# Kernel optimization log

Measured on AMD Instinct MI355X. Metric: run time of the kernel, lower is better.

Reference implementation:

```python
import jax, jax.numpy as jnp
import numpy as np

B = 256; M = 6; H = 448; INC = 448; EMB = 32; NHEAD = 8; DFF = 2048
OBS = 20; HOR = 30
D = EMB + 4 * NHEAD + INC      # transformer d_model = 512 (requires INC == hidden_dim)
LBUF = OBS + HOR               # 50-token buffer; index 49 is written but never read
HD = D // NHEAD
FUS_IN = D + 7 + INC           # fusion layer input = 71 + 2*hidden_dim


def _ln(x, g, b):
    mu = x.mean(-1, keepdims=True)
    var = ((x - mu) ** 2).mean(-1, keepdims=True)
    return (x - mu) * jax.lax.rsqrt(var + 1e-5) * g + b


def setup_inputs() -> dict:
    key = jax.random.key(0)
    ks = jax.random.split(key, 16)
    s = jnp.float32(0.02)
    n = lambda i, shp: jax.random.normal(ks[i], shp, dtype=jnp.float32)
    return {
        "feat_in": n(0, (B, 1, INC)),
        "loc_in": n(1, (B, M, 2)),
        "obs_trajs": n(2, (OBS, B, 2)),
        "W_emb": n(3, (2, EMB)) * s, "b_emb": jnp.zeros((EMB,)),
        "W_qkv": n(4, (D, 3 * D)) * s, "b_qkv": jnp.zeros((3 * D,)),
        "W_o": n(5, (D, D)) * s, "b_o": jnp.zeros((D,)),
        "W_ff1": n(6, (D, DFF)) * s, "b_ff1": jnp.zeros((DFF,)),
        "W_ff2": n(7, (DFF, D)) * s, "b_ff2": jnp.zeros((D,)),
        "ln1_g": jnp.ones((D,)), "ln1_b": jnp.zeros((D,)),
        "ln2_g": jnp.ones((D,)), "ln2_b": jnp.zeros((D,)),
        "W_fus": n(8, (FUS_IN, H)) * s, "b_fus": jnp.zeros((H,)),
        "W_out": n(9, (H, 2)) * s, "b_out": jnp.zeros((2,)),
    }


def reference(feat_in, loc_in, obs_trajs, W_emb, b_emb, W_qkv, b_qkv, W_o, b_o,
              W_ff1, b_ff1, W_ff2, b_ff2, ln1_g, ln1_b, ln2_g, ln2_b,
              W_fus, b_fus, W_out, b_out):
    feat = feat_in[:, 0]                                     # [B, INC]
    emb_obs = jax.nn.relu(obs_trajs @ W_emb + b_emb)         # [OBS, B, EMB]
    pos0 = jnp.zeros((LBUF, B, 2), feat.dtype).at[:OBS].set(obs_trajs)
    emb0 = jnp.zeros((LBUF, B, EMB), feat.dtype).at[:OBS].set(emb_obs)
    idxs = jnp.arange(OBS, OBS + HOR)
    scale = 1.0 / jnp.sqrt(jnp.float32(HD))
    rep = NHEAD // 2

    def run_sample(goal):                                    # goal: [B, 2]
        def step(carry, frame_idx):
            pos, emb = carry
            last = pos[frame_idx - 1]                        # [B, 2]
            dist = goal - last
            tcol = jnp.zeros((B, 1), feat.dtype) + frame_idx
            # order matches torch.cat: (emb, goal, last, dist, time, feat)
            extras = jnp.concatenate([jnp.tile(goal, (1, rep)), jnp.tile(last, (1, rep)),
                                      jnp.tile(dist, (1, rep)), jnp.tile(tcol, (1, NHEAD))], -1)
            x = jnp.concatenate([emb,
                                 jnp.broadcast_to(extras, (LBUF, B, 4 * NHEAD)),
                                 jnp.broadcast_to(feat, (LBUF, B, INC))], -1)   # [LBUF, B, D]
            qkv = x @ W_qkv + b_qkv
            q, k, v = jnp.split(qkv, 3, axis=-1)
            qh = q[frame_idx - 1].reshape(B, NHEAD, HD)      # only last query needed
            kh = k.reshape(LBUF, B, NHEAD, HD)
            vh = v.reshape(LBUF, B, NHEAD, HD)
            scores = jnp.einsum('bhd,lbhd->bhl', qh, kh) * scale
            valid = jnp.arange(LBUF) < frame_idx             # tokens 0..frame_idx-1 exist
            scores = jnp.where(valid[None, None, :], scores, -1e9)
            attn = jax.nn.softmax(scores, axis=-1)
            ctx = jnp.einsum('bhl,lbhd->bhd', attn, vh).reshape(B, D)
            a = ctx @ W_o + b_o
            x_last = x[frame_idx - 1]
            h1 = _ln(x_last + a, ln1_g, ln1_b)               # post-LN encoder layer (eval, no dropout)
            ff = jax.nn.relu(h1 @ W_ff1 + b_ff1) @ W_ff2 + b_ff2
            h2 = _ln(h1 + ff, ln2_g, ln2_b)
            fus = jnp.concatenate([h2, last, goal, dist, tcol, feat], -1)       # [B, FUS_IN]
            out = (fus @ W_fus + b_fus) @ W_out + b_out                         # [B, 2]
            pos = pos.at[frame_idx].set(out)
            emb = emb.at[frame_idx].set(jax.nn.relu(out @ W_emb + b_emb))
            return (pos, emb), out
        _, ys = jax.lax.scan(step, (pos0, emb0), idxs)
        return ys                                            # [HOR, B, 2]

    ys = jax.vmap(run_sample, in_axes=1)(loc_in)             # [M, HOR, B, 2]
    return ys.transpose(2, 0, 1, 3).reshape(B, M, HOR * 2)
```

## Files before the change

### kernel.cpp

```cpp
#include <hip/hip_runtime.h>
#include <math.h>

#define B_   256
#define N_   1536
#define OBS_ 20
#define HOR_ 30

typedef __bf16 bf16;
typedef bf16  bf16x8 __attribute__((ext_vector_type(8)));
typedef float f32x4  __attribute__((ext_vector_type(4)));

__global__ __launch_bounds__(256) void gemm_k(
    const float* __restrict__ A, int lda,
    const float* __restrict__ Bw, int ldb,
    float* __restrict__ C, bf16* __restrict__ Cb, int ldc,
    int K, const float* __restrict__ colBias)
{
    __shared__ float As[16][68];
    __shared__ float Bs[16][68];
    const int tid = threadIdx.x;
    const int tx = tid & 15, ty = tid >> 4;
    const int n0 = blockIdx.y * 64, j0 = blockIdx.x * 64;
    float acc[4][4] = {};
    const int a_kk = tid & 15, a_nn0 = tid >> 4;
    const int b_jj = tid & 63, b_kk0 = tid >> 6;
    for (int k0 = 0; k0 < K; k0 += 16) {
#pragma unroll
        for (int i = 0; i < 4; i++) {
            int nn = a_nn0 + 16 * i;
            As[a_kk][nn] = (k0 + a_kk < K) ? A[(size_t)(n0 + nn) * lda + k0 + a_kk] : 0.f;
        }
#pragma unroll
        for (int i = 0; i < 4; i++) {
            int kk = b_kk0 + 4 * i;
            Bs[kk][b_jj] = (k0 + kk < K) ? Bw[(size_t)(k0 + kk) * ldb + j0 + b_jj] : 0.f;
        }
        __syncthreads();
#pragma unroll
        for (int kk = 0; kk < 16; kk++) {
            float4 av = *(const float4*)&As[kk][ty * 4];
            float4 bv = *(const float4*)&Bs[kk][tx * 4];
            float aa[4] = {av.x, av.y, av.z, av.w};
            float bb[4] = {bv.x, bv.y, bv.z, bv.w};
#pragma unroll
            for (int i = 0; i < 4; i++)
#pragma unroll
                for (int j = 0; j < 4; j++) acc[i][j] += aa[i] * bb[j];
        }
        __syncthreads();
    }
#pragma unroll
    for (int i = 0; i < 4; i++) {
        int n = n0 + ty * 4 + i;
#pragma unroll
        for (int j = 0; j < 4; j++) {
            int jj = j0 + tx * 4 + j;
            float v = acc[i][j];
            if (colBias) v += colBias[jj];
            if (C)  C[(size_t)n * ldc + jj] = v;
            if (Cb) Cb[(size_t)n * ldc + jj] = (bf16)v;
        }
    }
}

__global__ void pack_k(const float* __restrict__ srcF, const bf16* __restrict__ srcB,
                       int srcRows, int KC, int J, int lds, bf16* __restrict__ dst)
{
    int idx = blockIdx.x * 256 + threadIdx.x;
    int total = (J / 16) * KC * 64;
    if (idx >= total) return;
    int lane = idx & 63;
    int kc = (idx >> 6) % KC;
    int jg = idx / (64 * KC);
    int k0 = kc * 32 + (lane >> 4) * 8;
    int col = jg * 16 + (lane & 15);
    bf16x8 v;
#pragma unroll
    for (int i = 0; i < 8; i++) {
        int r = k0 + i;
        float x = 0.f;
        if (r < srcRows) x = srcF ? srcF[(size_t)r * lds + col] : (float)srcB[(size_t)r * lds + col];
        v[i] = (bf16)x;
    }
    *(bf16x8*)&dst[(size_t)idx * 8] = v;
}

template<int KC>
__global__ __launch_bounds__(256) void fgemm_k(
    const bf16* __restrict__ A, int lda,
    const bf16* __restrict__ Bp,
    float* __restrict__ C, bf16* __restrict__ Cb, int ldc,
    const float* __restrict__ colBias,
    const float* __restrict__ rowMat, int ldRm,
    int doRelu)
{
    const int n0 = blockIdx.y * 32;
    const int j0g = blockIdx.x * 4;
    const int tid = threadIdx.x;
    const int w = tid >> 6, lane = tid & 63;
    const int quad = lane >> 4, m15 = lane & 15;
    const int r0 = (w & 1) * 16;
    const int cg = (w >> 1) * 2;
    const bf16* Arow = &A[(size_t)(n0 + r0 + m15) * lda + quad * 8];
    const bf16* B0 = &Bp[((size_t)(j0g + cg) * KC * 64 + lane) * 8];
    const bf16* B1 = &Bp[((size_t)(j0g + cg + 1) * KC * 64 + lane) * 8];
    f32x4 acc0 = {}, acc1 = {};
#pragma unroll 8
    for (int kc = 0; kc < KC; kc++) {
        bf16x8 af = *(const bf16x8*)&Arow[kc * 32];
        bf16x8 b0 = *(const bf16x8*)&B0[(size_t)kc * 512];
        bf16x8 b1 = *(const bf16x8*)&B1[(size_t)kc * 512];
        acc0 = __builtin_amdgcn_mfma_f32_16x16x32_bf16(af, b0, acc0, 0, 0, 0);
        acc1 = __builtin_amdgcn_mfma_f32_16x16x32_bf16(af, b1, acc1, 0, 0, 0);
    }
#pragma unroll
    for (int g = 0; g < 2; g++) {
        f32x4 a = g ? acc1 : acc0;
        int j = (j0g + cg + g) * 16 + m15;
        float cb = colBias ? colBias[j] : 0.f;
#pragma unroll
        for (int r = 0; r < 4; r++) {
            int n = n0 + r0 + quad * 4 + r;
            float v = a[r] + cb;
            if (rowMat) v += rowMat[(size_t)(n / 6) * ldRm + j];
            if (doRelu) v = fmaxf(v, 0.f);
            if (C)  C[(size_t)n * ldc + j] = v;
            if (Cb) Cb[(size_t)n * ldc + j] = (bf16)v;
        }
    }
}

__global__ __launch_bounds__(256) void emb_obs_k(
    const float* __restrict__ obs, const float* __restrict__ Wemb,
    const float* __restrict__ bemb, float* __restrict__ emb_obs)
{
    int tid = blockIdx.x * 256 + threadIdx.x;
    if (tid >= OBS_ * B_ * 32) return;
    int r = tid >> 5, e = tid & 31;
    float v = obs[r * 2] * Wemb[e] + obs[r * 2 + 1] * Wemb[32 + e] + bemb[e];
    emb_obs[tid] = fmaxf(v, 0.f);
}

__global__ __launch_bounds__(256) void weff_k(
    const float* __restrict__ Wqkv, const float* __restrict__ bqkv,
    float* __restrict__ Weff, float* __restrict__ WeffT)
{
    __shared__ float qrow[512];
    const int r = blockIdx.x;
    const int t = threadIdx.x;
    for (int j = t; j < 512; j += 256)
        qrow[j] = (r < 512) ? Wqkv[(size_t)r * 1536 + j] : bqkv[j];
    __syncthreads();
    const int h = t >> 5, c = t & 31;
    float acc = 0.f;
#pragma unroll 8
    for (int d = 0; d < 64; d++)
        acc += qrow[h * 64 + d] * Wqkv[(size_t)c * 1536 + 512 + h * 64 + d];
    Weff[(size_t)r * 256 + t] = acc;
    if (r < 64) WeffT[(size_t)t * 64 + r] = acc;
}

__global__ __launch_bounds__(256) void wov_k(
    const float* __restrict__ Wqkv, const float* __restrict__ Wo,
    bf16* __restrict__ WovCat)
{
    __shared__ float vrow[64];
    const int row = blockIdx.x;
    const int h = row >> 5, c = row & 31;
    const int t = threadIdx.x;
    if (t < 64) vrow[t] = Wqkv[(size_t)c * 1536 + 1024 + h * 64 + t];
    __syncthreads();
    for (int j = t; j < 512; j += 256) {
        float acc = 0.f;
#pragma unroll 8
        for (int d = 0; d < 64; d++)
            acc += vrow[d] * Wo[(size_t)(h * 64 + d) * 512 + j];
        WovCat[(size_t)row * 512 + j] = (bf16)acc;
    }
}

__global__ __launch_bounds__(256) void attn_k(
    const float* __restrict__ qp, const float* __restrict__ emb_obs,
    const float* __restrict__ emb_gen, bf16* __restrict__ ecA1b, int t)
{
    __shared__ float qp_s[256];
    __shared__ float emb_s[50 * 33];
    __shared__ float at_s[4][64];
    const int n = blockIdx.x, b = n / 6, tid = threadIdx.x;
    qp_s[tid] = qp[(size_t)n * 256 + tid];
    for (int idx = tid; idx < t * 32; idx += 256) {
        int l = idx >> 5, c = idx & 31;
        emb_s[l * 33 + c] = (l < OBS_) ? emb_obs[((size_t)l * B_ + b) * 32 + c]
                                       : emb_gen[((size_t)(l - OBS_) * N_ + n) * 32 + c];
    }
    __syncthreads();
    const int w = tid >> 6, lane = tid & 63;
#pragma unroll
    for (int hh = 0; hh < 2; hh++) {
        const int h = w * 2 + hh;
        float sc = -1e30f;
        if (lane < t) {
            float s_ = 0.f;
#pragma unroll 8
            for (int c = 0; c < 32; c++) s_ += emb_s[lane * 33 + c] * qp_s[h * 32 + c];
            sc = s_ * 0.125f;
        }
        float mx = sc;
#pragma unroll
        for (int o = 32; o > 0; o >>= 1) mx = fmaxf(mx, __shfl_xor(mx, o, 64));
        float e = (lane < t) ? __expf(sc - mx) : 0.f;
        float sm = e;
#pragma unroll
        for (int o = 32; o > 0; o >>= 1) sm += __shfl_xor(sm, o, 64);
        at_s[w][lane] = e / sm;
        if (lane < 32) {
            float ec = 0.f;
            for (int l = 0; l < t; l++) ec += at_s[w][l] * emb_s[l * 33 + lane];
            ecA1b[(size_t)n * 288 + h * 32 + lane] = (bf16)ec;
        }
    }
}

__global__ __launch_bounds__(512) void aln1_k(
    const bf16* __restrict__ A,
    const bf16* __restrict__ Bp,
    const float* __restrict__ featvO,
    const float* __restrict__ A1f,
    const float* __restrict__ feat,
    const float* __restrict__ g, const float* __restrict__ bt,
    float* __restrict__ h1f, bf16* __restrict__ h1b)
{
    __shared__ float redS[8][16];
    __shared__ float redQ[8][16];
    const int n0 = blockIdx.x * 16;
    const int tid = threadIdx.x;
    const int w = tid >> 6, lane = tid & 63;
    const int quad = lane >> 4, m15 = lane & 15;
    const bf16* Arow = &A[(size_t)(n0 + m15) * 288 + quad * 8];
    const bf16* Bb = &Bp[((size_t)(w * 4) * 9 * 64 + lane) * 8];
    f32x4 acc[4] = {};
#pragma unroll 3
    for (int kc = 0; kc < 9; kc++) {
        bf16x8 af = *(const bf16x8*)&Arow[kc * 32];
#pragma unroll
        for (int gi = 0; gi < 4; gi++) {
            bf16x8 bg = *(const bf16x8*)&Bb[(size_t)gi * 9 * 64 * 8 + (size_t)kc * 512];
            acc[gi] = __builtin_amdgcn_mfma_f32_16x16x32_bf16(af, bg, acc[gi], 0, 0, 0);
        }
    }
    float vv[4][4];
    float sS[4] = {}, sQ[4] = {};
#pragma unroll
    for (int gi = 0; gi < 4; gi++) {
        int j = (w * 4 + gi) * 16 + m15;
#pragma unroll
        for (int r = 0; r < 4; r++) {
            int n = n0 + quad * 4 + r;
            int b = n / 6;
            float x = (j < 64) ? A1f[(size_t)n * 64 + j] : feat[(size_t)b * 448 + (j - 64)];
            float v = acc[gi][r] + featvO[(size_t)b * 512 + j] + x;
            vv[gi][r] = v; sS[r] += v; sQ[r] += v * v;
        }
    }
#pragma unroll
    for (int o = 1; o < 16; o <<= 1) {
#pragma unroll
        for (int r = 0; r < 4; r++) { sS[r] += __shfl_xor(sS[r], o, 64); sQ[r] += __shfl_xor(sQ[r], o, 64); }
    }
    if (m15 == 0) {
#pragma unroll
        for (int r = 0; r < 4; r++) { redS[w][quad * 4 + r] = sS[r]; redQ[w][quad * 4 + r] = sQ[r]; }
    }
    __syncthreads();
    float mu[4], rs[4];
#pragma unroll
    for (int r = 0; r < 4; r++) {
        int row = quad * 4 + r;
        float s = 0.f, q = 0.f;
#pragma unroll
        for (int ww = 0; ww < 8; ww++) { s += redS[ww][row]; q += redQ[ww][row]; }
        mu[r] = s * (1.f / 512.f);
        float var = q * (1.f / 512.f) - mu[r] * mu[r];
        rs[r] = rsqrtf(var + 1e-5f);
    }
#pragma unroll
    for (int gi = 0; gi < 4; gi++) {
        int j = (w * 4 + gi) * 16 + m15;
        float gj = g[j], bj = bt[j];
#pragma unroll
        for (int r = 0; r < 4; r++) {
            int n = n0 + quad * 4 + r;
            float vn = (vv[gi][r] - mu[r]) * rs[r] * gj + bj;
            h1f[(size_t)n * 512 + j] = vn;
            h1b[(size_t)n * 512 + j] = (bf16)vn;
        }
    }
}

__global__ __launch_bounds__(256) void fusfin_k(
    const float* __restrict__ h1f, const float* __restrict__ ffB,
    const float* __restrict__ g2, const float* __restrict__ bt2,
    float* __restrict__ small5,
    const bf16* __restrict__ Bp,
    const float* __restrict__ feat_fus,
    const float* __restrict__ Wout, const float* __restrict__ bout,
    const float* __restrict__ Wemb, const float* __restrict__ bemb,
    const float* __restrict__ loc,
    const float* __restrict__ WeffT,
    const float* __restrict__ featqp,
    float* __restrict__ dout, float* __restrict__ emb_gen,
    float* __restrict__ A1f, bf16* __restrict__ ecA1b,
    float* __restrict__ qp, int s)
{
    __shared__ __attribute__((aligned(16))) bf16 h2s[16][552];
    __shared__ float red0[4][16], red1[4][16];
    __shared__ float osh[16][2];
    __shared__ __attribute__((aligned(16))) float A1s[16][64];
    const int n0 = blockIdx.x * 16;
    const int tid = threadIdx.x;

    {
        const int row = tid >> 4, li = tid & 15;
        const int n = n0 + row;
        float v32[32];
        float s_ = 0.f, sq = 0.f;
        const float* h1p = &h1f[(size_t)n * 512 + li * 32];
        const float* ffp = &ffB[(size_t)n * 512 + li * 32];
#pragma unroll
        for (int i4 = 0; i4 < 8; i4++) {
            float4 a4 = *(const float4*)&h1p[i4 * 4];
            float4 b4 = *(const float4*)&ffp[i4 * 4];
            float x0 = a4.x + b4.x, x1 = a4.y + b4.y, x2 = a4.z + b4.z, x3 = a4.w + b4.w;
            v32[i4 * 4 + 0] = x0; v32[i4 * 4 + 1] = x1; v32[i4 * 4 + 2] = x2; v32[i4 * 4 + 3] = x3;
            s_ += x0 + x1 + x2 + x3;
            sq += x0 * x0 + x1 * x1 + x2 * x2 + x3 * x3;
        }
#pragma unroll
        for (int o = 1; o < 16; o <<= 1) { s_ += __shfl_xor(s_, o, 64); sq += __shfl_xor(sq, o, 64); }
        float mu = s_ * (1.f / 512.f);
        float var = sq * (1.f / 512.f) - mu * mu;
        float rs = rsqrtf(var + 1e-5f);
#pragma unroll
        for (int i = 0; i < 32; i++) {
            int c = li * 32 + i;
            float vn = (v32[i] - mu) * rs * g2[c] + bt2[c];
            h2s[row][c] = (bf16)vn;
        }
        if (li == 0) {
#pragma unroll
            for (int sl = 0; sl < 32; sl++) {
                float vt = (sl < 7) ? small5[(size_t)n * 8 + sl] : 0.f;
                h2s[row][512 + sl] = (bf16)vt;
            }
        }
    }
    __syncthreads();

    const int w = tid >> 6, lane = tid & 63;
    const int quad = lane >> 4, m15 = lane & 15;
    {
        const bf16* Bb = &Bp[((size_t)(w * 7) * 17 * 64 + lane) * 8];
        f32x4 acc[7] = {};
#pragma unroll 2
        for (int kc = 0; kc < 17; kc++) {
            bf16x8 af = *(const bf16x8*)&h2s[m15][kc * 32 + quad * 8];
#pragma unroll
            for (int gi = 0; gi < 7; gi++) {
                bf16x8 bg = *(const bf16x8*)&Bb[(size_t)gi * 17 * 64 * 8 + (size_t)kc * 512];
                acc[gi] = __builtin_amdgcn_mfma_f32_16x16x32_bf16(af, bg, acc[gi], 0, 0, 0);
            }
        }
        float p0[4] = {}, p1[4] = {};
#pragma unroll
        for (int gi = 0; gi < 7; gi++) {
            int j = (w * 7 + gi) * 16 + m15;
            float w0 = Wout[j * 2], w1 = Wout[j * 2 + 1];
#pragma unroll
            for (int r = 0; r < 4; r++) {
                int n = n0 + quad * 4 + r;
                int b = n / 6;
                float v = acc[gi][r] + feat_fus[(size_t)b * 448 + j];
                p0[r] += v * w0; p1[r] += v * w1;
            }
        }
#pragma unroll
        for (int o = 1; o < 16; o <<= 1) {
#pragma unroll
            for (int r = 0; r < 4; r++) { p0[r] += __shfl_xor(p0[r], o, 64); p1[r] += __shfl_xor(p1[r], o, 64); }
        }
        if (m15 == 0) {
#pragma unroll
            for (int r = 0; r < 4; r++) { red0[w][quad * 4 + r] = p0[r]; red1[w][quad * 4 + r] = p1[r]; }
        }
    }
    __syncthreads();

    if (tid < 16) {
        const int row = tid;
        const int n = n0 + row, b = n / 6, m = n - b * 6;
        float o0 = red0[0][row] + red0[1][row] + red0[2][row] + red0[3][row] + bout[0];
        float o1 = red1[0][row] + red1[1][row] + red1[2][row] + red1[3][row] + bout[1];
        osh[row][0] = o0; osh[row][1] = o1;
        dout[(size_t)b * 360 + m * 60 + s * 2]     = o0;
        dout[(size_t)b * 360 + m * 60 + s * 2 + 1] = o1;
    }
    __syncthreads();

    {
        const int row = tid >> 4, li = tid & 15;
        const int n = n0 + row, b = n / 6, m = n - b * 6;
        float o0 = osh[row][0], o1 = osh[row][1];
        float g0 = loc[b * 12 + m * 2], g1 = loc[b * 12 + m * 2 + 1];
        float d0 = g0 - o0, d1 = g1 - o1;
        float tc = (float)(OBS_ + s + 1);
#pragma unroll
        for (int ii = 0; ii < 4; ii++) {
            int idx = li * 4 + ii;
            float val;
            if (idx < 32) {
                val = fmaxf(o0 * Wemb[idx] + o1 * Wemb[32 + idx] + bemb[idx], 0.f);
                emb_gen[((size_t)s * N_ + n) * 32 + idx] = val;
            } else {
                int c = idx - 32;
                val = (c < 8)  ? ((c & 1) ? g1 : g0)
                    : (c < 16) ? ((c & 1) ? o1 : o0)
                    : (c < 24) ? ((c & 1) ? d1 : d0)
                               : tc;
                ecA1b[(size_t)n * 288 + 256 + c] = (bf16)val;
            }
            A1s[row][idx] = val;
            A1f[(size_t)n * 64 + idx] = val;
        }
        if (li < 7) {
            float v2 = (li == 0) ? o0 : (li == 1) ? o1 : (li == 2) ? g0 : (li == 3) ? g1
                     : (li == 4) ? d0 : (li == 5) ? d1 : tc;
            small5[(size_t)n * 8 + li] = v2;
        }
    }
    __syncthreads();

    {
        const int c = tid;
        float accq[16];
#pragma unroll
        for (int r = 0; r < 16; r++) accq[r] = featqp[(size_t)((n0 + r) / 6) * 256 + c];
#pragma unroll 4
        for (int k4 = 0; k4 < 16; k4++) {
            float4 wv = *(const float4*)&WeffT[(size_t)c * 64 + k4 * 4];
#pragma unroll
            for (int r = 0; r < 16; r++) {
                float4 av = *(const float4*)&A1s[r][k4 * 4];
                float a = accq[r];
                a += av.x * wv.x; a += av.y * wv.y; a += av.z * wv.z; a += av.w * wv.w;
                accq[r] = a;
            }
        }
#pragma unroll
        for (int r = 0; r < 16; r++) qp[(size_t)(n0 + r) * 256 + c] = accq[r];
    }
}

__global__ __launch_bounds__(256) void init_k(
    const float* __restrict__ obs, const float* __restrict__ emb_obs,
    const float* __restrict__ loc, const float* __restrict__ Weff,
    const float* __restrict__ featqp,
    float* __restrict__ A1f, bf16* __restrict__ ecA1b,
    float* __restrict__ small5, float* __restrict__ qp)
{
    __shared__ float A1s[64];
    const int n = blockIdx.x, b = n / 6, m = n % 6, t = threadIdx.x;
    float o0 = obs[(19 * B_ + b) * 2], o1 = obs[(19 * B_ + b) * 2 + 1];
    float g0 = loc[b * 12 + m * 2], g1 = loc[b * 12 + m * 2 + 1];
    if (t < 32) {
        A1s[t] = emb_obs[((size_t)19 * B_ + b) * 32 + t];
    } else if (t < 64) {
        int c = t - 32; float d0 = g0 - o0, d1 = g1 - o1; float tc = 20.f;
        float v;
        if      (c < 8)  v = (c & 1) ? g1 : g0;
        else if (c < 16) v = (c & 1) ? o1 : o0;
        else if (c < 24) v = (c & 1) ? d1 : d0;
        else             v = tc;
        A1s[t] = v;
    }
    if (t < 7) {
        float d0 = g0 - o0, d1 = g1 - o1; float tc = 20.f;
        float v2 = (t==0)?o0:(t==1)?o1:(t==2)?g0:(t==3)?g1:(t==4)?d0:(t==5)?d1:tc;
        small5[n * 8 + t] = v2;
    }
    __syncthreads();
    if (t < 64) {
        A1f[(size_t)n * 64 + t] = A1s[t];
        if (t >= 32) ecA1b[(size_t)n * 288 + 256 + (t - 32)] = (bf16)A1s[t];
    }
    float acc = featqp[(size_t)b * 256 + t];
#pragma unroll 8
    for (int k = 0; k < 64; k++) acc += A1s[k] * Weff[k * 256 + t];
    qp[(size_t)n * 256 + t] = acc;
}

extern "C" void kernel_launch(void* const* d_in, const int* in_sizes, int n_in,
                              void* d_out_, int out_size, void* d_ws, size_t ws_size,
                              hipStream_t stream) {
    (void)in_sizes; (void)n_in; (void)out_size; (void)ws_size;
    const float* feat  = (const float*)d_in[0];
    const float* loc   = (const float*)d_in[1];
    const float* obs   = (const float*)d_in[2];
    const float* W_emb = (const float*)d_in[3];
    const float* b_emb = (const float*)d_in[4];
    const float* W_qkv = (const float*)d_in[5];
    const float* b_qkv = (const float*)d_in[6];
    const float* W_o   = (const float*)d_in[7];
    const float* b_o   = (const float*)d_in[8];
    const float* W_ff1 = (const float*)d_in[9];
    const float* b_ff1 = (const float*)d_in[10];
    const float* W_ff2 = (const float*)d_in[11];
    const float* b_ff2 = (const float*)d_in[12];
    const float* ln1_g = (const float*)d_in[13];
    const float* ln1_b = (const float*)d_in[14];
    const float* ln2_g = (const float*)d_in[15];
    const float* ln2_b = (const float*)d_in[16];
    const float* W_fus = (const float*)d_in[17];
    const float* b_fus = (const float*)d_in[18];
    const float* W_out = (const float*)d_in[19];
    const float* b_out = (const float*)d_in[20];
    float* dout = (float*)d_out_;

    float* ws = (float*)d_ws;
    float* Weff     = ws; ws += 513 * 256;
    float* WeffT    = ws; ws += 256 * 64;
    float* featqp   = ws; ws += 256 * 256;
    float* featv    = ws; ws += 256 * 512;
    float* featvO   = ws; ws += 256 * 512;
    float* feat_fus = ws; ws += 256 * 448;
    float* emb_obs  = ws; ws += OBS_ * B_ * 32;
    float* emb_gen  = ws; ws += HOR_ * N_ * 32;
    float* qp       = ws; ws += (size_t)N_ * 256;
    float* A1f      = ws; ws += (size_t)N_ * 64;
    float* small5   = ws; ws += (size_t)N_ * 8;
    float* h1f      = ws; ws += (size_t)N_ * 512;
    float* ffB      = ws; ws += (size_t)N_ * 512;
    bf16* WovCat = (bf16*)ws; ws += (320 * 512) / 2;
    bf16* BpA    = (bf16*)ws; ws += (32 * 9 * 512) / 2;
    bf16* BpF1   = (bf16*)ws; ws += (128 * 16 * 512) / 2;
    bf16* BpF2   = (bf16*)ws; ws += (32 * 64 * 512) / 2;
    bf16* BpFus  = (bf16*)ws; ws += (28 * 17 * 512) / 2;
    bf16* ecA1b  = (bf16*)ws; ws += ((size_t)N_ * 288) / 2;
    bf16* h1b    = (bf16*)ws; ws += ((size_t)N_ * 512) / 2;
    bf16* f1b    = (bf16*)ws; ws += ((size_t)N_ * 2048) / 2;

    emb_obs_k<<<dim3(640), dim3(256), 0, stream>>>(obs, W_emb, b_emb, emb_obs);
    weff_k<<<dim3(513), dim3(256), 0, stream>>>(W_qkv, b_qkv, Weff, WeffT);
    gemm_k<<<dim3(4, 4), dim3(256), 0, stream>>>(feat, 448, Weff + 64 * 256, 256,
        featqp, nullptr, 256, 448, Weff + 512 * 256);
    wov_k<<<dim3(256), dim3(256), 0, stream>>>(W_qkv, W_o, WovCat);
    gemm_k<<<dim3(8, 4), dim3(256), 0, stream>>>(feat, 448, W_qkv + 64 * 1536 + 1024, 1536,
        featv, nullptr, 512, 448, b_qkv + 1024);
    gemm_k<<<dim3(8, 4), dim3(256), 0, stream>>>(featv, 512, W_o, 512,
        featvO, nullptr, 512, 512, b_o);
    gemm_k<<<dim3(8, 1), dim3(256), 0, stream>>>(W_qkv + 32 * 1536 + 1024, 1536, W_o, 512,
        featv, WovCat + 256 * 512, 512, 512, nullptr);
    gemm_k<<<dim3(7, 4), dim3(256), 0, stream>>>(feat, 448, W_fus + 519 * 448, 448,
        feat_fus, nullptr, 448, 448, b_fus);
    pack_k<<<dim3(72),  dim3(256), 0, stream>>>(nullptr, WovCat, 288, 9,  512,  512,  BpA);
    pack_k<<<dim3(512), dim3(256), 0, stream>>>(W_ff1, nullptr, 512, 16, 2048, 2048, BpF1);
    pack_k<<<dim3(512), dim3(256), 0, stream>>>(W_ff2, nullptr, 2048, 64, 512, 512,  BpF2);
    pack_k<<<dim3(120), dim3(256), 0, stream>>>(W_fus, nullptr, 519, 17, 448,  448,  BpFus);
    init_k<<<dim3(N_), dim3(256), 0, stream>>>(obs, emb_obs, loc, Weff, featqp,
        A1f, ecA1b, small5, qp);

    for (int s = 0; s < HOR_; s++) {
        attn_k<<<dim3(N_), dim3(256), 0, stream>>>(qp, emb_obs, emb_gen, ecA1b, OBS_ + s);
        aln1_k<<<dim3(N_ / 16), dim3(512), 0, stream>>>(ecA1b, BpA, featvO, A1f, feat,
            ln1_g, ln1_b, h1f, h1b);
        fgemm_k<16><<<dim3(32, 48), dim3(256), 0, stream>>>(h1b, 512, BpF1,
            nullptr, f1b, 2048, b_ff1, nullptr, 0, 1);
        fgemm_k<64><<<dim3(8, 48), dim3(256), 0, stream>>>(f1b, 2048, BpF2,
            ffB, nullptr, 512, b_ff2, nullptr, 0, 0);
        fusfin_k<<<dim3(N_ / 16), dim3(256), 0, stream>>>(h1f, ffB, ln2_g, ln2_b, small5,
            BpFus, feat_fus, W_out, b_out, W_emb, b_emb, loc, WeffT, featqp,
            dout, emb_gen, A1f, ecA1b, qp, s);
    }
}
```

Measured before the change: 3.042 ms.

## Merge prologue kernels into two launches and widen fusfin to 512 threads

The twelve setup kernels (embedding, Weff, Wov, small GEMMs, weight packing) are folded into two block-indexed launches. The small FP32 GEMM now uses 32-row tiles with register prefetch of the next K slice. The per-step fusfin kernel goes from 256 to 512 threads, halving per-thread work in the LayerNorm, fusion MFMA and qp update phases. The aim is to cut launch overhead and raise parallelism in a per-step kernel that launches only 96 blocks. In exchange it adds divergent branching in the merged kernels and removes the K-bounds guard in the GEMM loads.

```diff
diff --git a/kernel.cpp b/kernel.cpp
--- a/kernel.cpp
+++ b/kernel.cpp
@@ -10,48 +10,53 @@
 typedef bf16  bf16x8 __attribute__((ext_vector_type(8)));
 typedef float f32x4  __attribute__((ext_vector_type(4)));
 
-__global__ __launch_bounds__(256) void gemm_k(
+__device__ __forceinline__ void dev_gemm(
     const float* __restrict__ A, int lda,
     const float* __restrict__ Bw, int ldb,
     float* __restrict__ C, bf16* __restrict__ Cb, int ldc,
-    int K, const float* __restrict__ colBias)
-{
-    __shared__ float As[16][68];
-    __shared__ float Bs[16][68];
+    int K, const float* __restrict__ colBias,
+    int by, int bx, float* smem)
+{
+    float (*As)[36] = (float(*)[36])smem;
+    float (*Bs)[68] = (float(*)[68])(smem + 16 * 36);
     const int tid = threadIdx.x;
+    const int n0 = by * 32, j0 = bx * 64;
+    const int a_k = tid & 15, a_r = tid >> 4;
+    const int b_j = tid & 63, b_k = tid >> 6;
     const int tx = tid & 15, ty = tid >> 4;
-    const int n0 = blockIdx.y * 64, j0 = blockIdx.x * 64;
-    float acc[4][4] = {};
-    const int a_kk = tid & 15, a_nn0 = tid >> 4;
-    const int b_jj = tid & 63, b_kk0 = tid >> 6;
+    float acc[2][4] = {};
+    float pa0 = A[(size_t)(n0 + a_r) * lda + a_k];
+    float pa1 = A[(size_t)(n0 + a_r + 16) * lda + a_k];
+    float pb[4];
+#pragma unroll
+    for (int i = 0; i < 4; i++) pb[i] = Bw[(size_t)(b_k + 4 * i) * ldb + j0 + b_j];
     for (int k0 = 0; k0 < K; k0 += 16) {
-#pragma unroll
-        for (int i = 0; i < 4; i++) {
-            int nn = a_nn0 + 16 * i;
-            As[a_kk][nn] = (k0 + a_kk < K) ? A[(size_t)(n0 + nn) * lda + k0 + a_kk] : 0.f;
-        }
-#pragma unroll
-        for (int i = 0; i < 4; i++) {
-            int kk = b_kk0 + 4 * i;
-            Bs[kk][b_jj] = (k0 + kk < K) ? Bw[(size_t)(k0 + kk) * ldb + j0 + b_jj] : 0.f;
-        }
+        As[a_k][a_r] = pa0;
+        As[a_k][a_r + 16] = pa1;
+#pragma unroll
+        for (int i = 0; i < 4; i++) Bs[b_k + 4 * i][b_j] = pb[i];
         __syncthreads();
+        if (k0 + 16 < K) {
+            pa0 = A[(size_t)(n0 + a_r) * lda + k0 + 16 + a_k];
+            pa1 = A[(size_t)(n0 + a_r + 16) * lda + k0 + 16 + a_k];
+#pragma unroll
+            for (int i = 0; i < 4; i++)
+                pb[i] = Bw[(size_t)(k0 + 16 + b_k + 4 * i) * ldb + j0 + b_j];
+        }
 #pragma unroll
         for (int kk = 0; kk < 16; kk++) {
-            float4 av = *(const float4*)&As[kk][ty * 4];
+            float a0 = As[kk][ty * 2];
+            float a1 = As[kk][ty * 2 + 1];
             float4 bv = *(const float4*)&Bs[kk][tx * 4];
-            float aa[4] = {av.x, av.y, av.z, av.w};
             float bb[4] = {bv.x, bv.y, bv.z, bv.w};
 #pragma unroll
-            for (int i = 0; i < 4; i++)
-#pragma unroll
-                for (int j = 0; j < 4; j++) acc[i][j] += aa[i] * bb[j];
+            for (int j = 0; j < 4; j++) { acc[0][j] += a0 * bb[j]; acc[1][j] += a1 * bb[j]; }
         }
         __syncthreads();
     }
 #pragma unroll
-    for (int i = 0; i < 4; i++) {
-        int n = n0 + ty * 4 + i;
+    for (int i = 0; i < 2; i++) {
+        int n = n0 + ty * 2 + i;
 #pragma unroll
         for (int j = 0; j < 4; j++) {
             int jj = j0 + tx * 4 + j;
@@ -63,10 +68,11 @@
     }
 }
 
-__global__ void pack_k(const float* __restrict__ srcF, const bf16* __restrict__ srcB,
-                       int srcRows, int KC, int J, int lds, bf16* __restrict__ dst)
-{
-    int idx = blockIdx.x * 256 + threadIdx.x;
+__device__ __forceinline__ void dev_pack(
+    int bi, const float* __restrict__ srcF, const bf16* __restrict__ srcB,
+    int srcRows, int KC, int J, int lds, bf16* __restrict__ dst)
+{
+    int idx = bi * 256 + threadIdx.x;
     int total = (J / 16) * KC * 64;
     if (idx >= total) return;
     int lane = idx & 63;
@@ -83,6 +89,117 @@
         v[i] = (bf16)x;
     }
     *(bf16x8*)&dst[(size_t)idx * 8] = v;
+}
+
+__device__ __forceinline__ void dev_emb_obs(
+    int bi, const float* __restrict__ obs, const float* __restrict__ Wemb,
+    const float* __restrict__ bemb, float* __restrict__ emb_obs)
+{
+    int tid = bi * 256 + threadIdx.x;
+    if (tid >= OBS_ * B_ * 32) return;
+    int r = tid >> 5, e = tid & 31;
+    float v = obs[r * 2] * Wemb[e] + obs[r * 2 + 1] * Wemb[32 + e] + bemb[e];
+    emb_obs[tid] = fmaxf(v, 0.f);
+}
+
+__device__ __forceinline__ void dev_weff(
+    int r, const float* __restrict__ Wqkv, const float* __restrict__ bqkv,
+    float* __restrict__ Weff, float* __restrict__ WeffT, float* smem)
+{
+    float* qrow = smem;
+    const int t = threadIdx.x;
+    for (int j = t; j < 512; j += 256)
+        qrow[j] = (r < 512) ? Wqkv[(size_t)r * 1536 + j] : bqkv[j];
+    __syncthreads();
+    const int h = t >> 5, c = t & 31;
+    float acc = 0.f;
+#pragma unroll 8
+    for (int d = 0; d < 64; d++)
+        acc += qrow[h * 64 + d] * Wqkv[(size_t)c * 1536 + 512 + h * 64 + d];
+    Weff[(size_t)r * 256 + t] = acc;
+    if (r < 64) WeffT[(size_t)t * 64 + r] = acc;
+}
+
+__device__ __forceinline__ void dev_wov(
+    int row, const float* __restrict__ Wqkv, const float* __restrict__ Wo,
+    bf16* __restrict__ WovCat, float* smem)
+{
+    float* vrow = smem;
+    const int h = row >> 5, c = row & 31;
+    const int t = threadIdx.x;
+    if (t < 64) vrow[t] = Wqkv[(size_t)c * 1536 + 1024 + h * 64 + t];
+    __syncthreads();
+    for (int j = t; j < 512; j += 256) {
+        float acc = 0.f;
+#pragma unroll 8
+        for (int d = 0; d < 64; d++)
+            acc += vrow[d] * Wo[(size_t)(h * 64 + d) * 512 + j];
+        WovCat[(size_t)row * 512 + j] = (bf16)acc;
+    }
+}
+
+__global__ __launch_bounds__(256) void prologue1_k(
+    const float* __restrict__ obs, const float* __restrict__ Wemb,
+    const float* __restrict__ bemb, float* __restrict__ emb_obs,
+    const float* __restrict__ Wqkv, const float* __restrict__ bqkv,
+    float* __restrict__ Weff, float* __restrict__ WeffT,
+    const float* __restrict__ Wo, bf16* __restrict__ WovCat,
+    const float* __restrict__ feat, float* __restrict__ featv,
+    const float* __restrict__ Wfus, const float* __restrict__ bfus,
+    float* __restrict__ feat_fus,
+    const float* __restrict__ Wff1, bf16* __restrict__ BpF1,
+    const float* __restrict__ Wff2, bf16* __restrict__ BpF2,
+    bf16* __restrict__ BpFus)
+{
+    __shared__ __attribute__((aligned(16))) float smem[16 * 36 + 16 * 68];
+    const int b = blockIdx.x;
+    if (b < 640) {
+        dev_emb_obs(b, obs, Wemb, bemb, emb_obs);
+    } else if (b < 1153) {
+        dev_weff(b - 640, Wqkv, bqkv, Weff, WeffT, smem);
+    } else if (b < 1409) {
+        dev_wov(b - 1153, Wqkv, Wo, WovCat, smem);
+    } else if (b < 1473) {
+        int i = b - 1409;
+        dev_gemm(feat, 448, Wqkv + 64 * 1536 + 1024, 1536,
+                 featv, nullptr, 512, 448, bqkv + 1024, i >> 3, i & 7, smem);
+    } else if (b < 1489) {
+        int i = b - 1473;
+        dev_gemm(Wqkv + 32 * 1536 + 1024, 1536, Wo, 512,
+                 nullptr, WovCat + 256 * 512, 512, 512, nullptr, i >> 3, i & 7, smem);
+    } else if (b < 1545) {
+        int i = b - 1489;
+        dev_gemm(feat, 448, Wfus + 519 * 448, 448,
+                 feat_fus, nullptr, 448, 448, bfus, i / 7, i % 7, smem);
+    } else if (b < 2057) {
+        dev_pack(b - 1545, Wff1, nullptr, 512, 16, 2048, 2048, BpF1);
+    } else if (b < 2569) {
+        dev_pack(b - 2057, Wff2, nullptr, 2048, 64, 512, 512, BpF2);
+    } else {
+        dev_pack(b - 2569, Wfus, nullptr, 519, 17, 448, 448, BpFus);
+    }
+}
+
+__global__ __launch_bounds__(256) void prologue2_k(
+    const float* __restrict__ feat, const float* __restrict__ Weff,
+    float* __restrict__ featqp,
+    const float* __restrict__ featv, const float* __restrict__ Wo,
+    const float* __restrict__ b_o, float* __restrict__ featvO,
+    const bf16* __restrict__ WovCat, bf16* __restrict__ BpA)
+{
+    __shared__ __attribute__((aligned(16))) float smem[16 * 36 + 16 * 68];
+    const int b = blockIdx.x;
+    if (b < 32) {
+        int i = b;
+        dev_gemm(feat, 448, Weff + 64 * 256, 256,
+                 featqp, nullptr, 256, 448, Weff + 512 * 256, i >> 2, i & 3, smem);
+    } else if (b < 96) {
+        int i = b - 32;
+        dev_gemm(featv, 512, Wo, 512,
+                 featvO, nullptr, 512, 512, b_o, i >> 3, i & 7, smem);
+    } else {
+        dev_pack(b - 96, nullptr, WovCat, 288, 9, 512, 512, BpA);
+    }
 }
 
 template<int KC>
@@ -130,55 +247,6 @@
     }
 }
 
-__global__ __launch_bounds__(256) void emb_obs_k(
-    const float* __restrict__ obs, const float* __restrict__ Wemb,
-    const float* __restrict__ bemb, float* __restrict__ emb_obs)
-{
-    int tid = blockIdx.x * 256 + threadIdx.x;
-    if (tid >= OBS_ * B_ * 32) return;
-    int r = tid >> 5, e = tid & 31;
-    float v = obs[r * 2] * Wemb[e] + obs[r * 2 + 1] * Wemb[32 + e] + bemb[e];
-    emb_obs[tid] = fmaxf(v, 0.f);
-}
-
-__global__ __launch_bounds__(256) void weff_k(
-    const float* __restrict__ Wqkv, const float* __restrict__ bqkv,
-    float* __restrict__ Weff, float* __restrict__ WeffT)
-{
-    __shared__ float qrow[512];
-    const int r = blockIdx.x;
-    const int t = threadIdx.x;
-    for (int j = t; j < 512; j += 256)
-        qrow[j] = (r < 512) ? Wqkv[(size_t)r * 1536 + j] : bqkv[j];
-    __syncthreads();
-    const int h = t >> 5, c = t & 31;
-    float acc = 0.f;
-#pragma unroll 8
-    for (int d = 0; d < 64; d++)
-        acc += qrow[h * 64 + d] * Wqkv[(size_t)c * 1536 + 512 + h * 64 + d];
-    Weff[(size_t)r * 256 + t] = acc;
-    if (r < 64) WeffT[(size_t)t * 64 + r] = acc;
-}
-
-__global__ __launch_bounds__(256) void wov_k(
-    const float* __restrict__ Wqkv, const float* __restrict__ Wo,
-    bf16* __restrict__ WovCat)
-{
-    __shared__ float vrow[64];
-    const int row = blockIdx.x;
-    const int h = row >> 5, c = row & 31;
-    const int t = threadIdx.x;
-    if (t < 64) vrow[t] = Wqkv[(size_t)c * 1536 + 1024 + h * 64 + t];
-    __syncthreads();
-    for (int j = t; j < 512; j += 256) {
-        float acc = 0.f;
-#pragma unroll 8
-        for (int d = 0; d < 64; d++)
-            acc += vrow[d] * Wo[(size_t)(h * 64 + d) * 512 + j];
-        WovCat[(size_t)row * 512 + j] = (bf16)acc;
-    }
-}
-
 __global__ __launch_bounds__(256) void attn_k(
     const float* __restrict__ qp, const float* __restrict__ emb_obs,
     const float* __restrict__ emb_gen, bf16* __restrict__ ecA1b, int t)
@@ -297,7 +365,7 @@
     }
 }
 
-__global__ __launch_bounds__(256) void fusfin_k(
+__global__ __launch_bounds__(512) void fusfin_k(
     const float* __restrict__ h1f, const float* __restrict__ ffB,
     const float* __restrict__ g2, const float* __restrict__ bt2,
     float* __restrict__ small5,
@@ -313,38 +381,37 @@
     float* __restrict__ qp, int s)
 {
     __shared__ __attribute__((aligned(16))) bf16 h2s[16][552];
-    __shared__ float red0[4][16], red1[4][16];
+    __shared__ float red0[8][16], red1[8][16];
     __shared__ float osh[16][2];
     __shared__ __attribute__((aligned(16))) float A1s[16][64];
     const int n0 = blockIdx.x * 16;
     const int tid = threadIdx.x;
 
     {
-        const int row = tid >> 4, li = tid & 15;
+        const int row = tid >> 5, li = tid & 31;
         const int n = n0 + row;
-        float v32[32];
+        float v16[16];
         float s_ = 0.f, sq = 0.f;
-        const float* h1p = &h1f[(size_t)n * 512 + li * 32];
-        const float* ffp = &ffB[(size_t)n * 512 + li * 32];
-#pragma unroll
-        for (int i4 = 0; i4 < 8; i4++) {
+        const float* h1p = &h1f[(size_t)n * 512 + li * 16];
+        const float* ffp = &ffB[(size_t)n * 512 + li * 16];
+#pragma unroll
+        for (int i4 = 0; i4 < 4; i4++) {
             float4 a4 = *(const float4*)&h1p[i4 * 4];
             float4 b4 = *(const float4*)&ffp[i4 * 4];
             float x0 = a4.x + b4.x, x1 = a4.y + b4.y, x2 = a4.z + b4.z, x3 = a4.w + b4.w;
-            v32[i4 * 4 + 0] = x0; v32[i4 * 4 + 1] = x1; v32[i4 * 4 + 2] = x2; v32[i4 * 4 + 3] = x3;
+            v16[i4 * 4 + 0] = x0; v16[i4 * 4 + 1] = x1; v16[i4 * 4 + 2] = x2; v16[i4 * 4 + 3] = x3;
             s_ += x0 + x1 + x2 + x3;
             sq += x0 * x0 + x1 * x1 + x2 * x2 + x3 * x3;
         }
 #pragma unroll
-        for (int o = 1; o < 16; o <<= 1) { s_ += __shfl_xor(s_, o, 64); sq += __shfl_xor(sq, o, 64); }
+        for (int o = 1; o < 32; o <<= 1) { s_ += __shfl_xor(s_, o, 64); sq += __shfl_xor(sq, o, 64); }
         float mu = s_ * (1.f / 512.f);
         float var = sq * (1.f / 512.f) - mu * mu;
         float rs = rsqrtf(var + 1e-5f);
 #pragma unroll
-        for (int i = 0; i < 32; i++) {
-            int c = li * 32 + i;
-            float vn = (v32[i] - mu) * rs * g2[c] + bt2[c];
-            h2s[row][c] = (bf16)vn;
+        for (int i = 0; i < 16; i++) {
+            int c = li * 16 + i;
+            h2s[row][c] = (bf16)((v16[i] - mu) * rs * g2[c] + bt2[c]);
         }
         if (li == 0) {
 #pragma unroll
@@ -359,28 +426,33 @@
     const int w = tid >> 6, lane = tid & 63;
     const int quad = lane >> 4, m15 = lane & 15;
     {
-        const bf16* Bb = &Bp[((size_t)(w * 7) * 17 * 64 + lane) * 8];
-        f32x4 acc[7] = {};
+        const int ng = (w < 4) ? 4 : 3;
+        f32x4 acc[4] = {};
 #pragma unroll 2
         for (int kc = 0; kc < 17; kc++) {
             bf16x8 af = *(const bf16x8*)&h2s[m15][kc * 32 + quad * 8];
 #pragma unroll
-            for (int gi = 0; gi < 7; gi++) {
-                bf16x8 bg = *(const bf16x8*)&Bb[(size_t)gi * 17 * 64 * 8 + (size_t)kc * 512];
-                acc[gi] = __builtin_amdgcn_mfma_f32_16x16x32_bf16(af, bg, acc[gi], 0, 0, 0);
+            for (int gi = 0; gi < 4; gi++) {
+                if (gi < ng) {
+                    int g = w + gi * 8;
+                    bf16x8 bg = *(const bf16x8*)&Bp[(((size_t)g * 17 + kc) * 64 + lane) * 8];
+                    acc[gi] = __builtin_amdgcn_mfma_f32_16x16x32_bf16(af, bg, acc[gi], 0, 0, 0);
+                }
             }
         }
         float p0[4] = {}, p1[4] = {};
 #pragma unroll
-        for (int gi = 0; gi < 7; gi++) {
-            int j = (w * 7 + gi) * 16 + m15;
-            float w0 = Wout[j * 2], w1 = Wout[j * 2 + 1];
-#pragma unroll
-            for (int r = 0; r < 4; r++) {
-                int n = n0 + quad * 4 + r;
-                int b = n / 6;
-                float v = acc[gi][r] + feat_fus[(size_t)b * 448 + j];
-                p0[r] += v * w0; p1[r] += v * w1;
+        for (int gi = 0; gi < 4; gi++) {
+            if (gi < ng) {
+                int j = (w + gi * 8) * 16 + m15;
+                float w0 = Wout[j * 2], w1 = Wout[j * 2 + 1];
+#pragma unroll
+                for (int r = 0; r < 4; r++) {
+                    int n = n0 + quad * 4 + r;
+                    int b = n / 6;
+                    float v = acc[gi][r] + feat_fus[(size_t)b * 448 + j];
+                    p0[r] += v * w0; p1[r] += v * w1;
+                }
             }
         }
 #pragma unroll
@@ -398,8 +470,9 @@
     if (tid < 16) {
         const int row = tid;
         const int n = n0 + row, b = n / 6, m = n - b * 6;
-        float o0 = red0[0][row] + red0[1][row] + red0[2][row] + red0[3][row] + bout[0];
-        float o1 = red1[0][row] + red1[1][row] + red1[2][row] + red1[3][row] + bout[1];
+        float o0 = bout[0], o1 = bout[1];
+#pragma unroll
+        for (int ww = 0; ww < 8; ww++) { o0 += red0[ww][row]; o1 += red1[ww][row]; }
         osh[row][0] = o0; osh[row][1] = o1;
         dout[(size_t)b * 360 + m * 60 + s * 2]     = o0;
         dout[(size_t)b * 360 + m * 60 + s * 2 + 1] = o1;
@@ -407,15 +480,15 @@
     __syncthreads();
 
     {
-        const int row = tid >> 4, li = tid & 15;
+        const int row = tid >> 5, li = tid & 31;
         const int n = n0 + row, b = n / 6, m = n - b * 6;
         float o0 = osh[row][0], o1 = osh[row][1];
         float g0 = loc[b * 12 + m * 2], g1 = loc[b * 12 + m * 2 + 1];
         float d0 = g0 - o0, d1 = g1 - o1;
         float tc = (float)(OBS_ + s + 1);
 #pragma unroll
-        for (int ii = 0; ii < 4; ii++) {
-            int idx = li * 4 + ii;
+        for (int ii = 0; ii < 2; ii++) {
+            int idx = li * 2 + ii;
             float val;
             if (idx < 32) {
                 val = fmaxf(o0 * Wemb[idx] + o1 * Wemb[32 + idx] + bemb[idx], 0.f);
@@ -440,23 +513,24 @@
     __syncthreads();
 
     {
-        const int c = tid;
-        float accq[16];
-#pragma unroll
-        for (int r = 0; r < 16; r++) accq[r] = featqp[(size_t)((n0 + r) / 6) * 256 + c];
+        const int c = tid & 255;
+        const int rh = (tid >> 8) * 8;
+        float accq[8];
+#pragma unroll
+        for (int r = 0; r < 8; r++) accq[r] = featqp[(size_t)((n0 + rh + r) / 6) * 256 + c];
 #pragma unroll 4
         for (int k4 = 0; k4 < 16; k4++) {
             float4 wv = *(const float4*)&WeffT[(size_t)c * 64 + k4 * 4];
 #pragma unroll
-            for (int r = 0; r < 16; r++) {
-                float4 av = *(const float4*)&A1s[r][k4 * 4];
+            for (int r = 0; r < 8; r++) {
+                float4 av = *(const float4*)&A1s[rh + r][k4 * 4];
                 float a = accq[r];
                 a += av.x * wv.x; a += av.y * wv.y; a += av.z * wv.z; a += av.w * wv.w;
                 accq[r] = a;
             }
         }
 #pragma unroll
-        for (int r = 0; r < 16; r++) qp[(size_t)(n0 + r) * 256 + c] = accq[r];
+        for (int r = 0; r < 8; r++) qp[(size_t)(n0 + rh + r) * 256 + c] = accq[r];
     }
 }
 
@@ -548,23 +622,11 @@
     bf16* h1b    = (bf16*)ws; ws += ((size_t)N_ * 512) / 2;
     bf16* f1b    = (bf16*)ws; ws += ((size_t)N_ * 2048) / 2;
 
-    emb_obs_k<<<dim3(640), dim3(256), 0, stream>>>(obs, W_emb, b_emb, emb_obs);
-    weff_k<<<dim3(513), dim3(256), 0, stream>>>(W_qkv, b_qkv, Weff, WeffT);
-    gemm_k<<<dim3(4, 4), dim3(256), 0, stream>>>(feat, 448, Weff + 64 * 256, 256,
-        featqp, nullptr, 256, 448, Weff + 512 * 256);
-    wov_k<<<dim3(256), dim3(256), 0, stream>>>(W_qkv, W_o, WovCat);
-    gemm_k<<<dim3(8, 4), dim3(256), 0, stream>>>(feat, 448, W_qkv + 64 * 1536 + 1024, 1536,
-        featv, nullptr, 512, 448, b_qkv + 1024);
-    gemm_k<<<dim3(8, 4), dim3(256), 0, stream>>>(featv, 512, W_o, 512,
-        featvO, nullptr, 512, 512, b_o);
-    gemm_k<<<dim3(8, 1), dim3(256), 0, stream>>>(W_qkv + 32 * 1536 + 1024, 1536, W_o, 512,
-        featv, WovCat + 256 * 512, 512, 512, nullptr);
-    gemm_k<<<dim3(7, 4), dim3(256), 0, stream>>>(feat, 448, W_fus + 519 * 448, 448,
-        feat_fus, nullptr, 448, 448, b_fus);
-    pack_k<<<dim3(72),  dim3(256), 0, stream>>>(nullptr, WovCat, 288, 9,  512,  512,  BpA);
-    pack_k<<<dim3(512), dim3(256), 0, stream>>>(W_ff1, nullptr, 512, 16, 2048, 2048, BpF1);
-    pack_k<<<dim3(512), dim3(256), 0, stream>>>(W_ff2, nullptr, 2048, 64, 512, 512,  BpF2);
-    pack_k<<<dim3(120), dim3(256), 0, stream>>>(W_fus, nullptr, 519, 17, 448,  448,  BpFus);
+    prologue1_k<<<dim3(2688), dim3(256), 0, stream>>>(
+        obs, W_emb, b_emb, emb_obs, W_qkv, b_qkv, Weff, WeffT, W_o, WovCat,
+        feat, featv, W_fus, b_fus, feat_fus, W_ff1, BpF1, W_ff2, BpF2, BpFus);
+    prologue2_k<<<dim3(168), dim3(256), 0, stream>>>(
+        feat, Weff, featqp, featv, W_o, b_o, featvO, WovCat, BpA);
     init_k<<<dim3(N_), dim3(256), 0, stream>>>(obs, emb_obs, loc, Weff, featqp,
         A1f, ecA1b, small5, qp);
 
@@ -576,7 +638,7 @@
             nullptr, f1b, 2048, b_ff1, nullptr, 0, 1);
         fgemm_k<64><<<dim3(8, 48), dim3(256), 0, stream>>>(f1b, 2048, BpF2,
             ffB, nullptr, 512, b_ff2, nullptr, 0, 0);
-        fusfin_k<<<dim3(N_ / 16), dim3(256), 0, stream>>>(h1f, ffB, ln2_g, ln2_b, small5,
+        fusfin_k<<<dim3(N_ / 16), dim3(512), 0, stream>>>(h1f, ffB, ln2_g, ln2_b, small5,
             BpFus, feat_fus, W_out, b_out, W_emb, b_emb, loc, WeffT, featqp,
             dout, emb_gen, A1f, ecA1b, qp, s);
     }
```

Result: faster. 2.888 ms (-5.1%).
